# Optimization experiments

Hardware: AMD Instinct MI355X
Metric: run time of the kernel (lower is better)

The kernel has to match this reference:

```python
import jax, jax.numpy as jnp
import numpy as np

N_NODES = 50000
N_EDGES = 800000
IN_CH = 128
HID_CH = 128   # factor(2) * out_channels(64)
OUT_CH = 64


def setup_inputs() -> dict:
    key = jax.random.key(0)
    k_x, k_e, k_w1, k_w2 = jax.random.split(key, 4)
    x = jax.random.normal(k_x, (N_NODES, IN_CH), dtype=jnp.float32)
    edge_index = jax.random.randint(k_e, (2, N_EDGES), 0, N_NODES, dtype=jnp.int32)
    # GCNConv weights (Glorot) and biases, layer1: in->2*out, layer2: 2*out->out
    s1 = float(np.sqrt(6.0 / (IN_CH + HID_CH)))
    s2 = float(np.sqrt(6.0 / (HID_CH + OUT_CH)))
    W1 = jax.random.uniform(k_w1, (IN_CH, HID_CH), jnp.float32, -s1, s1)
    b1 = jnp.zeros((HID_CH,), jnp.float32)
    W2 = jax.random.uniform(k_w2, (HID_CH, OUT_CH), jnp.float32, -s2, s2)
    b2 = jnp.zeros((OUT_CH,), jnp.float32)
    return {"x": x, "edge_index": edge_index, "W1": W1, "b1": b1, "W2": W2, "b2": b2}


def reference(x, edge_index, W1, b1, W2, b2):
    N = x.shape[0]
    src, dst = edge_index[0], edge_index[1]
    # add self loops (PyG GCNConv default)
    loop = jnp.arange(N, dtype=edge_index.dtype)
    src2 = jnp.concatenate([src, loop])
    dst2 = jnp.concatenate([dst, loop])
    # symmetric normalization D^-1/2 (A+I) D^-1/2
    deg = jax.ops.segment_sum(jnp.ones_like(src2, dtype=x.dtype), dst2, num_segments=N)
    deg_inv_sqrt = jnp.where(deg > 0, jax.lax.rsqrt(jnp.maximum(deg, 1e-12)), 0.0)
    norm = deg_inv_sqrt[src2] * deg_inv_sqrt[dst2]  # [E+N]

    def gcn_conv(h, W, b):
        h = h @ W                                   # [N, C_out]
        msg = h[src2] * norm[:, None]               # gather + scale
        agg = jax.ops.segment_sum(msg, dst2, num_segments=N)  # scatter-add
        return agg + b

    h = jax.nn.relu(gcn_conv(x, W1, b1))
    h = jax.nn.relu(gcn_conv(h, W2, b2))
    return h
```

## Files before the change

kernel.cpp:

```cpp
#include <hip/hip_runtime.h>
#include <math.h>

#define NN 50000
#define NE 800000
#define NB 391
#define CAP 4096
#define CHUNK 4096

typedef __attribute__((ext_vector_type(8))) short s8v;
typedef __attribute__((ext_vector_type(8))) unsigned short u16x8;
typedef __attribute__((ext_vector_type(4))) float f4v;

__device__ inline short bf16_rtn(float f) {
  unsigned u = __builtin_bit_cast(unsigned, f);
  u = (u + 0x7FFFu + ((u >> 16) & 1u)) >> 16;
  return (short)u;
}
__device__ inline float bf16_to_f(unsigned short h) {
  unsigned u = ((unsigned)h) << 16;
  return __builtin_bit_cast(float, u);
}

__global__ __launch_bounds__(512) void k_bucketA(const int* __restrict__ src,
                                                 const int* __restrict__ dst,
                                                 int* __restrict__ bcnt,
                                                 unsigned* __restrict__ ebuf, int E) {
  __shared__ int h[NB], lofs[NB], gbase[NB], lcur[NB];
  __shared__ unsigned staged[CHUNK];
  const int tid = threadIdx.x;
  const int e0 = blockIdx.x * CHUNK;
  const int nE = min(CHUNK, E - e0);
  for (int i = tid; i < NB; i += 512) { h[i] = 0; lcur[i] = 0; }
  __syncthreads();
  for (int i = tid; i < nE; i += 512) atomicAdd(&h[dst[e0 + i] >> 7], 1);
  __syncthreads();
  if (tid < 64) {
    int carry = 0;
    for (int c = 0; c < 7; ++c) {
      int idx = c * 64 + tid;
      int v = (idx < NB) ? h[idx] : 0;
      int s = v;
#pragma unroll
      for (int o = 1; o < 64; o <<= 1) {
        int t = __shfl_up(s, o);
        if (tid >= o) s += t;
      }
      if (idx < NB) lofs[idx] = carry + s - v;
      carry += __shfl(s, 63);
    }
  }
  __syncthreads();
  for (int i = tid; i < NB; i += 512)
    gbase[i] = h[i] ? (i * CAP + atomicAdd(&bcnt[i], h[i])) : 0;
  __syncthreads();
  for (int i = tid; i < nE; i += 512) {
    int d = dst[e0 + i];
    int s = src[e0 + i];
    int b = d >> 7;
    int pos = lofs[b] + atomicAdd(&lcur[b], 1);
    staged[pos] = ((unsigned)b << 23) | ((unsigned)(d & 127) << 16) | (unsigned)s;
  }
  __syncthreads();
  for (int i = tid; i < nE; i += 512) {
    unsigned v = staged[i];
    int b = v >> 23;
    ebuf[gbase[b] + (i - lofs[b])] = v;
  }
}

__global__ __launch_bounds__(256) void k_bucketB(const unsigned* __restrict__ ebuf,
                                                 const int* __restrict__ bcnt,
                                                 unsigned short* __restrict__ col,
                                                 int* __restrict__ rps,
                                                 int* __restrict__ rpe,
                                                 float* __restrict__ dinv) {
  __shared__ int h[128], ofs[128], lc[128];
  const int tid = threadIdx.x;
  const int b = blockIdx.x;
  const int base = b * CAP;
  const int cntE = bcnt[b];
  const int node0 = b << 7;
  const int nloc = min(128, NN - node0);
  if (tid < 128) { h[tid] = 0; lc[tid] = 0; }
  __syncthreads();
  for (int i = tid; i < cntE; i += 256) atomicAdd(&h[(ebuf[base + i] >> 16) & 127], 1);
  __syncthreads();
  if (tid < 64) {
    int carry = 0;
    for (int c = 0; c < 2; ++c) {
      int idx = c * 64 + tid;
      int v = h[idx];
      int s = v;
#pragma unroll
      for (int o = 1; o < 64; o <<= 1) {
        int t = __shfl_up(s, o);
        if (tid >= o) s += t;
      }
      ofs[idx] = carry + s - v;
      carry += __shfl(s, 63);
    }
  }
  __syncthreads();
  if (tid < nloc) {
    rps[node0 + tid] = base + ofs[tid];
    rpe[node0 + tid] = base + ofs[tid] + h[tid];
    dinv[node0 + tid] = rsqrtf((float)h[tid] + 1.0f);
  }
  __syncthreads();
  for (int i = tid; i < cntE; i += 256) {
    unsigned v = ebuf[base + i];
    int l = (v >> 16) & 127;
    int p = atomicAdd(&lc[l], 1);
    col[base + ofs[l] + p] = (unsigned short)(v & 0xFFFFu);
  }
}

template <int N>
__global__ __launch_bounds__(512) void k_gemm_mfma(const float* __restrict__ X,
                                                   const float* __restrict__ W,
                                                   unsigned short* __restrict__ H,
                                                   int* __restrict__ bcnt,
                                                   int M) {
  constexpr int NT = N / 16;
  constexpr int NSLOT = 4 * NT * 64;
  __shared__ short s_hi[NSLOT * 8];
  __shared__ short s_lo[NSLOT * 8];
  const int tid = threadIdx.x;

  if (blockIdx.x == 0)
    for (int i = tid; i < NB; i += 512) bcnt[i] = 0;

  for (int slot = tid; slot < NSLOT; slot += 512) {
    int lane = slot & 63;
    int frag = slot >> 6;
    int nt = frag % NT;
    int kt = frag / NT;
    int colb = nt * 16 + (lane & 15);
    int kb = kt * 32 + (lane >> 4) * 8;
    s8v hi, lo;
#pragma unroll
    for (int j = 0; j < 8; ++j) {
      float w = W[(size_t)(kb + j) * N + colb];
      short h = bf16_rtn(w);
      hi[j] = h;
      lo[j] = bf16_rtn(w - bf16_to_f((unsigned short)h));
    }
    *(s8v*)&s_hi[slot * 8] = hi;
    *(s8v*)&s_lo[slot * 8] = lo;
  }
  __syncthreads();

  const int wave = tid >> 6, lane = tid & 63;
  const int row0 = blockIdx.x * 128 + wave * 16;
  int arow = row0 + (lane & 15);
  if (arow >= M) arow = M - 1;
  const float* xr = X + (size_t)arow * 128 + (lane >> 4) * 8;

  f4v acc[NT];
#pragma unroll
  for (int nt = 0; nt < NT; ++nt) acc[nt] = (f4v){0.f, 0.f, 0.f, 0.f};

#pragma unroll
  for (int kt = 0; kt < 4; ++kt) {
    float4 a0 = *(const float4*)(xr + kt * 32);
    float4 a1 = *(const float4*)(xr + kt * 32 + 4);
    float af[8] = {a0.x, a0.y, a0.z, a0.w, a1.x, a1.y, a1.z, a1.w};
    s8v ah, al;
#pragma unroll
    for (int j = 0; j < 8; ++j) {
      short h = bf16_rtn(af[j]);
      ah[j] = h;
      al[j] = bf16_rtn(af[j] - bf16_to_f((unsigned short)h));
    }
#pragma unroll
    for (int nt = 0; nt < NT; ++nt) {
      int base = ((kt * NT + nt) * 64 + lane) * 8;
      s8v bh = *(const s8v*)&s_hi[base];
      s8v bl = *(const s8v*)&s_lo[base];
      acc[nt] = __builtin_amdgcn_mfma_f32_16x16x32_bf16(ah, bh, acc[nt], 0, 0, 0);
      acc[nt] = __builtin_amdgcn_mfma_f32_16x16x32_bf16(ah, bl, acc[nt], 0, 0, 0);
      acc[nt] = __builtin_amdgcn_mfma_f32_16x16x32_bf16(al, bh, acc[nt], 0, 0, 0);
    }
  }

  const int orow = row0 + (lane >> 4) * 4;
  const int ocol = lane & 15;
#pragma unroll
  for (int nt = 0; nt < NT; ++nt)
#pragma unroll
    for (int r = 0; r < 4; ++r)
      if (orow + r < M)
        H[(size_t)(orow + r) * N + nt * 16 + ocol] =
            (unsigned short)bf16_rtn(acc[nt][r]);
}

__global__ __launch_bounds__(256) void k_agg1_gemm2(
    const unsigned short* __restrict__ H1, const unsigned short* __restrict__ col,
    const int* __restrict__ rps, const int* __restrict__ rpe,
    const float* __restrict__ dinv, const float* __restrict__ b1,
    const float* __restrict__ W2, unsigned short* __restrict__ H2) {
  __shared__ unsigned short s_w2[1024 * 8];
  __shared__ unsigned short s_a1[16 * 136];
  const int tid = threadIdx.x;

  for (int slot = tid; slot < 1024; slot += 256) {
    int lane = slot & 63;
    int frag = slot >> 6;
    int nt = frag & 3;
    int kt = frag >> 2;
    int colb = nt * 16 + (lane & 15);
    int kb = kt * 32 + (lane >> 4) * 8;
    u16x8 hi;
#pragma unroll
    for (int j = 0; j < 8; ++j)
      hi[j] = (unsigned short)bf16_rtn(W2[(size_t)(kb + j) * 64 + colb]);
    *(u16x8*)&s_w2[slot * 8] = hi;
  }

  const int ln = tid >> 4;
  const int node = blockIdx.x * 16 + ln;
  const int cg = (tid & 15) * 8;
  float di = dinv[node];
  float acc[8];
  u16x8 hv = *(const u16x8*)(H1 + (size_t)node * 128 + cg);
#pragma unroll
  for (int q = 0; q < 8; ++q) acc[q] = bf16_to_f(hv[q]) * di;
  int j = rps[node];
  int end = rpe[node];
  for (; j + 4 <= end; j += 4) {
    int s0 = col[j + 0], s1 = col[j + 1], s2 = col[j + 2], s3 = col[j + 3];
    float w0 = dinv[s0], w1 = dinv[s1], w2 = dinv[s2], w3 = dinv[s3];
    u16x8 a = *(const u16x8*)(H1 + (size_t)s0 * 128 + cg);
    u16x8 b = *(const u16x8*)(H1 + (size_t)s1 * 128 + cg);
    u16x8 c = *(const u16x8*)(H1 + (size_t)s2 * 128 + cg);
    u16x8 d = *(const u16x8*)(H1 + (size_t)s3 * 128 + cg);
#pragma unroll
    for (int q = 0; q < 8; ++q)
      acc[q] += bf16_to_f(a[q]) * w0 + bf16_to_f(b[q]) * w1 +
                bf16_to_f(c[q]) * w2 + bf16_to_f(d[q]) * w3;
  }
  for (; j < end; ++j) {
    int s = col[j];
    float w = dinv[s];
    u16x8 a = *(const u16x8*)(H1 + (size_t)s * 128 + cg);
#pragma unroll
    for (int q = 0; q < 8; ++q) acc[q] += bf16_to_f(a[q]) * w;
  }
  float4 bv0 = *(const float4*)(b1 + cg);
  float4 bv1 = *(const float4*)(b1 + cg + 4);
  float r[8];
  r[0] = acc[0] * di + bv0.x; r[1] = acc[1] * di + bv0.y;
  r[2] = acc[2] * di + bv0.z; r[3] = acc[3] * di + bv0.w;
  r[4] = acc[4] * di + bv1.x; r[5] = acc[5] * di + bv1.y;
  r[6] = acc[6] * di + bv1.z; r[7] = acc[7] * di + bv1.w;
  u16x8 o;
#pragma unroll
  for (int q = 0; q < 8; ++q)
    o[q] = (unsigned short)bf16_rtn(r[q] > 0.f ? r[q] : 0.f);
  *(u16x8*)&s_a1[ln * 136 + cg] = o;
  __syncthreads();

  const int wave = tid >> 6, lane = tid & 63;
  f4v cacc = (f4v){0.f, 0.f, 0.f, 0.f};
#pragma unroll
  for (int kt = 0; kt < 4; ++kt) {
    s8v ah = __builtin_bit_cast(
        s8v, *(const u16x8*)&s_a1[(lane & 15) * 136 + kt * 32 + (lane >> 4) * 8]);
    s8v bh = *(const s8v*)&s_w2[((kt * 4 + wave) * 64 + lane) * 8];
    cacc = __builtin_amdgcn_mfma_f32_16x16x32_bf16(ah, bh, cacc, 0, 0, 0);
  }
  const int node0 = blockIdx.x * 16;
  const int orow = (lane >> 4) * 4;
  const int ocol = lane & 15;
#pragma unroll
  for (int rr = 0; rr < 4; ++rr) {
    int nd = node0 + orow + rr;
    H2[(size_t)nd * 64 + wave * 16 + ocol] =
        (unsigned short)bf16_rtn(cacc[rr] * dinv[nd]);
  }
}

__global__ __launch_bounds__(256) void k_agg2(const unsigned short* __restrict__ H,
                                              const unsigned short* __restrict__ col,
                                              const int* __restrict__ rps,
                                              const int* __restrict__ rpe,
                                              const float* __restrict__ dinv,
                                              const float* __restrict__ bias,
                                              float* __restrict__ out, int n) {
  int node = blockIdx.x * 32 + threadIdx.x / 8;
  int cg = (threadIdx.x % 8) * 8;
  if (node >= n) return;
  float di = dinv[node];
  float acc[8];
  u16x8 hv = *(const u16x8*)(H + (size_t)node * 64 + cg);
#pragma unroll
  for (int q = 0; q < 8; ++q) acc[q] = bf16_to_f(hv[q]);
  int j = rps[node];
  int end = rpe[node];
  for (; j + 4 <= end; j += 4) {
    int s0 = col[j + 0], s1 = col[j + 1], s2 = col[j + 2], s3 = col[j + 3];
    u16x8 a = *(const u16x8*)(H + (size_t)s0 * 64 + cg);
    u16x8 b = *(const u16x8*)(H + (size_t)s1 * 64 + cg);
    u16x8 c = *(const u16x8*)(H + (size_t)s2 * 64 + cg);
    u16x8 d = *(const u16x8*)(H + (size_t)s3 * 64 + cg);
#pragma unroll
    for (int q = 0; q < 8; ++q)
      acc[q] += bf16_to_f(a[q]) + bf16_to_f(b[q]) + bf16_to_f(c[q]) + bf16_to_f(d[q]);
  }
  for (; j < end; ++j) {
    u16x8 a = *(const u16x8*)(H + (size_t)col[j] * 64 + cg);
#pragma unroll
    for (int q = 0; q < 8; ++q) acc[q] += bf16_to_f(a[q]);
  }
  float4 bv0 = *(const float4*)(bias + cg);
  float4 bv1 = *(const float4*)(bias + cg + 4);
  float r[8];
  r[0] = acc[0] * di + bv0.x; r[1] = acc[1] * di + bv0.y;
  r[2] = acc[2] * di + bv0.z; r[3] = acc[3] * di + bv0.w;
  r[4] = acc[4] * di + bv1.x; r[5] = acc[5] * di + bv1.y;
  r[6] = acc[6] * di + bv1.z; r[7] = acc[7] * di + bv1.w;
#pragma unroll
  for (int q = 0; q < 8; ++q) r[q] = r[q] > 0.f ? r[q] : 0.f;
  *(float4*)(out + (size_t)node * 64 + cg) = make_float4(r[0], r[1], r[2], r[3]);
  *(float4*)(out + (size_t)node * 64 + cg + 4) = make_float4(r[4], r[5], r[6], r[7]);
}

extern "C" void kernel_launch(void* const* d_in, const int* in_sizes, int n_in,
                              void* d_out, int out_size, void* d_ws, size_t ws_size,
                              hipStream_t stream) {
  const float* x  = (const float*)d_in[0];
  const int*   ei = (const int*)d_in[1];
  const float* W1 = (const float*)d_in[2];
  const float* b1 = (const float*)d_in[3];
  const float* W2 = (const float*)d_in[4];
  const float* b2 = (const float*)d_in[5];
  float* out = (float*)d_out;

  const int N = NN, E = NE;
  const int* src = ei;
  const int* dst = ei + E;

  char* ws = (char*)d_ws;
  size_t off = 0;
  auto carve = [&](size_t bytes) -> void* {
    void* p = ws + off;
    off = (off + bytes + 255) & ~(size_t)255;
    return p;
  };
  int*            bcnt = (int*)carve((size_t)NB * 4);
  unsigned short* col  = (unsigned short*)carve((size_t)NB * CAP * 2);
  int*            rps  = (int*)carve((size_t)N * 4);
  int*            rpe  = (int*)carve((size_t)N * 4);
  float*          dinv = (float*)carve((size_t)N * 4);
  unsigned short* H2   = (unsigned short*)carve((size_t)N * 64 * 2);
  unsigned short* H1   = (unsigned short*)carve((size_t)N * 128 * 2);
  unsigned*       ebuf = (unsigned*)carve((size_t)NB * CAP * 4);

  const int GB = (NN + 127) / 128;

  k_gemm_mfma<128><<<GB, 512, 0, stream>>>(x, W1, H1, bcnt, N);

  k_bucketA<<<(E + CHUNK - 1) / CHUNK, 512, 0, stream>>>(src, dst, bcnt, ebuf, E);
  k_bucketB<<<NB, 256, 0, stream>>>(ebuf, bcnt, col, rps, rpe, dinv);

  k_agg1_gemm2<<<NN / 16, 256, 0, stream>>>(H1, col, rps, rpe, dinv, b1, W2, H2);

  k_agg2<<<(N + 31) / 32, 256, 0, stream>>>(H2, col, rps, rpe, dinv, b2, out, N);
}
```

Measured before the change: 87.95 us.

## Fuse layer-1 GEMM with edge bucketing and drop global bucket atomics

Merges the first-layer MFMA GEMM and the edge bucketing pass into one launch, using a block-index split so GEMM blocks and bucketing blocks run concurrently. Bucketing blocks no longer claim space in each bucket through global atomics. Each block instead writes its locally sorted chunk together with per-bucket counts and offsets, and the second pass gathers each bucket's runs by a prefix scan and binary search into shared memory. This removes one kernel launch and the contention on the global counters, and avoids a separate zeroing step. The cost is extra per-slice metadata traffic and a larger shared-memory footprint in the fused kernel, which may reduce occupancy for the GEMM blocks.

```diff
diff --git a/kernel.cpp b/kernel.cpp
--- a/kernel.cpp
+++ b/kernel.cpp
@@ -6,6 +6,8 @@
 #define NB 391
 #define CAP 4096
 #define CHUNK 4096
+#define NSLICE 196
+#define GB 391
 
 typedef __attribute__((ext_vector_type(8))) short s8v;
 typedef __attribute__((ext_vector_type(8))) unsigned short u16x8;
@@ -21,69 +23,176 @@
   return __builtin_bit_cast(float, u);
 }
 
-__global__ __launch_bounds__(512) void k_bucketA(const int* __restrict__ src,
-                                                 const int* __restrict__ dst,
-                                                 int* __restrict__ bcnt,
-                                                 unsigned* __restrict__ ebuf, int E) {
-  __shared__ int h[NB], lofs[NB], gbase[NB], lcur[NB];
-  __shared__ unsigned staged[CHUNK];
+__global__ __launch_bounds__(512) void k_gemm1_bucketA(
+    const float* __restrict__ X, const float* __restrict__ W,
+    unsigned short* __restrict__ H,
+    const int* __restrict__ src, const int* __restrict__ dst,
+    int* __restrict__ cnts, int* __restrict__ lofsg,
+    unsigned* __restrict__ ebuf2, int M, int E) {
+  __shared__ char smem[65536];
   const int tid = threadIdx.x;
-  const int e0 = blockIdx.x * CHUNK;
-  const int nE = min(CHUNK, E - e0);
-  for (int i = tid; i < NB; i += 512) { h[i] = 0; lcur[i] = 0; }
-  __syncthreads();
-  for (int i = tid; i < nE; i += 512) atomicAdd(&h[dst[e0 + i] >> 7], 1);
-  __syncthreads();
-  if (tid < 64) {
-    int carry = 0;
-    for (int c = 0; c < 7; ++c) {
-      int idx = c * 64 + tid;
-      int v = (idx < NB) ? h[idx] : 0;
-      int s = v;
-#pragma unroll
-      for (int o = 1; o < 64; o <<= 1) {
-        int t = __shfl_up(s, o);
-        if (tid >= o) s += t;
-      }
-      if (idx < NB) lofs[idx] = carry + s - v;
-      carry += __shfl(s, 63);
-    }
-  }
-  __syncthreads();
-  for (int i = tid; i < NB; i += 512)
-    gbase[i] = h[i] ? (i * CAP + atomicAdd(&bcnt[i], h[i])) : 0;
-  __syncthreads();
-  for (int i = tid; i < nE; i += 512) {
-    int d = dst[e0 + i];
-    int s = src[e0 + i];
-    int b = d >> 7;
-    int pos = lofs[b] + atomicAdd(&lcur[b], 1);
-    staged[pos] = ((unsigned)b << 23) | ((unsigned)(d & 127) << 16) | (unsigned)s;
-  }
-  __syncthreads();
-  for (int i = tid; i < nE; i += 512) {
-    unsigned v = staged[i];
-    int b = v >> 23;
-    ebuf[gbase[b] + (i - lofs[b])] = v;
-  }
-}
-
-__global__ __launch_bounds__(256) void k_bucketB(const unsigned* __restrict__ ebuf,
-                                                 const int* __restrict__ bcnt,
+
+  if (blockIdx.x < GB) {
+    constexpr int NT = 8;
+    constexpr int NSLOT = 4 * NT * 64;
+    short* s_hi = (short*)smem;
+    short* s_lo = (short*)(smem + 32768);
+
+    for (int slot = tid; slot < NSLOT; slot += 512) {
+      int lane = slot & 63;
+      int frag = slot >> 6;
+      int nt = frag % NT;
+      int kt = frag / NT;
+      int colb = nt * 16 + (lane & 15);
+      int kb = kt * 32 + (lane >> 4) * 8;
+      s8v hi, lo;
+#pragma unroll
+      for (int j = 0; j < 8; ++j) {
+        float w = W[(size_t)(kb + j) * 128 + colb];
+        short h = bf16_rtn(w);
+        hi[j] = h;
+        lo[j] = bf16_rtn(w - bf16_to_f((unsigned short)h));
+      }
+      *(s8v*)&s_hi[slot * 8] = hi;
+      *(s8v*)&s_lo[slot * 8] = lo;
+    }
+    __syncthreads();
+
+    const int wave = tid >> 6, lane = tid & 63;
+    const int row0 = blockIdx.x * 128 + wave * 16;
+    int arow = row0 + (lane & 15);
+    if (arow >= M) arow = M - 1;
+    const float* xr = X + (size_t)arow * 128 + (lane >> 4) * 8;
+
+    f4v acc[NT];
+#pragma unroll
+    for (int nt = 0; nt < NT; ++nt) acc[nt] = (f4v){0.f, 0.f, 0.f, 0.f};
+
+#pragma unroll
+    for (int kt = 0; kt < 4; ++kt) {
+      float4 a0 = *(const float4*)(xr + kt * 32);
+      float4 a1 = *(const float4*)(xr + kt * 32 + 4);
+      float af[8] = {a0.x, a0.y, a0.z, a0.w, a1.x, a1.y, a1.z, a1.w};
+      s8v ah, al;
+#pragma unroll
+      for (int j = 0; j < 8; ++j) {
+        short h = bf16_rtn(af[j]);
+        ah[j] = h;
+        al[j] = bf16_rtn(af[j] - bf16_to_f((unsigned short)h));
+      }
+#pragma unroll
+      for (int nt = 0; nt < NT; ++nt) {
+        int base = ((kt * NT + nt) * 64 + lane) * 8;
+        s8v bh = *(const s8v*)&s_hi[base];
+        s8v bl = *(const s8v*)&s_lo[base];
+        acc[nt] = __builtin_amdgcn_mfma_f32_16x16x32_bf16(ah, bh, acc[nt], 0, 0, 0);
+        acc[nt] = __builtin_amdgcn_mfma_f32_16x16x32_bf16(ah, bl, acc[nt], 0, 0, 0);
+        acc[nt] = __builtin_amdgcn_mfma_f32_16x16x32_bf16(al, bh, acc[nt], 0, 0, 0);
+      }
+    }
+
+    const int orow = row0 + (lane >> 4) * 4;
+    const int ocol = lane & 15;
+#pragma unroll
+    for (int nt = 0; nt < NT; ++nt)
+#pragma unroll
+      for (int r = 0; r < 4; ++r)
+        if (orow + r < M)
+          H[(size_t)(orow + r) * 128 + nt * 16 + ocol] =
+              (unsigned short)bf16_rtn(acc[nt][r]);
+  } else {
+    int* h    = (int*)smem;
+    int* lofs = (int*)(smem + 1600);
+    int* lcur = (int*)(smem + 3200);
+    unsigned* staged = (unsigned*)(smem + 4800);
+    const int k = blockIdx.x - GB;
+    const int e0 = k * CHUNK;
+    const int nE = min(CHUNK, E - e0);
+    for (int i = tid; i < NB; i += 512) { h[i] = 0; lcur[i] = 0; }
+    __syncthreads();
+    for (int i = tid; i < nE; i += 512) atomicAdd(&h[dst[e0 + i] >> 7], 1);
+    __syncthreads();
+    if (tid < 64) {
+      int carry = 0;
+      for (int c = 0; c < 7; ++c) {
+        int idx = c * 64 + tid;
+        int v = (idx < NB) ? h[idx] : 0;
+        int s = v;
+#pragma unroll
+        for (int o = 1; o < 64; o <<= 1) {
+          int t = __shfl_up(s, o);
+          if (tid >= o) s += t;
+        }
+        if (idx < NB) lofs[idx] = carry + s - v;
+        carry += __shfl(s, 63);
+      }
+    }
+    __syncthreads();
+    for (int i = tid; i < nE; i += 512) {
+      int d = dst[e0 + i];
+      int s = src[e0 + i];
+      int b = d >> 7;
+      int pos = lofs[b] + atomicAdd(&lcur[b], 1);
+      staged[pos] = ((unsigned)(d & 127) << 16) | (unsigned)s;
+    }
+    __syncthreads();
+    for (int i = tid; i < nE; i += 512) ebuf2[e0 + i] = staged[i];
+    for (int i = tid; i < NB; i += 512) {
+      cnts[(size_t)k * NB + i] = h[i];
+      lofsg[(size_t)k * NB + i] = lofs[i];
+    }
+  }
+}
+
+__global__ __launch_bounds__(256) void k_bucketB(const unsigned* __restrict__ ebuf2,
+                                                 const int* __restrict__ cnts,
+                                                 const int* __restrict__ lofsg,
                                                  unsigned short* __restrict__ col,
                                                  int* __restrict__ rps,
                                                  int* __restrict__ rpe,
                                                  float* __restrict__ dinv) {
+  __shared__ int scnt[NSLICE], sofs[NSLICE], runstart[NSLICE + 1];
   __shared__ int h[128], ofs[128], lc[128];
+  __shared__ unsigned estage[CAP];
   const int tid = threadIdx.x;
   const int b = blockIdx.x;
   const int base = b * CAP;
-  const int cntE = bcnt[b];
   const int node0 = b << 7;
   const int nloc = min(128, NN - node0);
+  for (int k = tid; k < NSLICE; k += 256) {
+    scnt[k] = cnts[(size_t)k * NB + b];
+    sofs[k] = lofsg[(size_t)k * NB + b];
+  }
   if (tid < 128) { h[tid] = 0; lc[tid] = 0; }
   __syncthreads();
-  for (int i = tid; i < cntE; i += 256) atomicAdd(&h[(ebuf[base + i] >> 16) & 127], 1);
+  if (tid < 64) {
+    int carry = 0;
+    for (int c = 0; c < 4; ++c) {
+      int idx = c * 64 + tid;
+      int v = (idx < NSLICE) ? scnt[idx] : 0;
+      int s = v;
+#pragma unroll
+      for (int o = 1; o < 64; o <<= 1) {
+        int t = __shfl_up(s, o);
+        if (tid >= o) s += t;
+      }
+      if (idx < NSLICE) runstart[idx] = carry + s - v;
+      carry += __shfl(s, 63);
+    }
+    if (tid == 0) runstart[NSLICE] = carry;
+  }
+  __syncthreads();
+  const int cntE = runstart[NSLICE];
+  for (int i = tid; i < cntE; i += 256) {
+    int lo = 0, hi = NSLICE - 1;
+    while (lo < hi) {
+      int mid = (lo + hi + 1) >> 1;
+      if (runstart[mid] <= i) lo = mid; else hi = mid - 1;
+    }
+    estage[i] = ebuf2[lo * CHUNK + sofs[lo] + (i - runstart[lo])];
+  }
+  __syncthreads();
+  for (int i = tid; i < cntE; i += 256) atomicAdd(&h[(estage[i] >> 16) & 127], 1);
   __syncthreads();
   if (tid < 64) {
     int carry = 0;
@@ -108,90 +217,11 @@
   }
   __syncthreads();
   for (int i = tid; i < cntE; i += 256) {
-    unsigned v = ebuf[base + i];
+    unsigned v = estage[i];
     int l = (v >> 16) & 127;
     int p = atomicAdd(&lc[l], 1);
     col[base + ofs[l] + p] = (unsigned short)(v & 0xFFFFu);
   }
-}
-
-template <int N>
-__global__ __launch_bounds__(512) void k_gemm_mfma(const float* __restrict__ X,
-                                                   const float* __restrict__ W,
-                                                   unsigned short* __restrict__ H,
-                                                   int* __restrict__ bcnt,
-                                                   int M) {
-  constexpr int NT = N / 16;
-  constexpr int NSLOT = 4 * NT * 64;
-  __shared__ short s_hi[NSLOT * 8];
-  __shared__ short s_lo[NSLOT * 8];
-  const int tid = threadIdx.x;
-
-  if (blockIdx.x == 0)
-    for (int i = tid; i < NB; i += 512) bcnt[i] = 0;
-
-  for (int slot = tid; slot < NSLOT; slot += 512) {
-    int lane = slot & 63;
-    int frag = slot >> 6;
-    int nt = frag % NT;
-    int kt = frag / NT;
-    int colb = nt * 16 + (lane & 15);
-    int kb = kt * 32 + (lane >> 4) * 8;
-    s8v hi, lo;
-#pragma unroll
-    for (int j = 0; j < 8; ++j) {
-      float w = W[(size_t)(kb + j) * N + colb];
-      short h = bf16_rtn(w);
-      hi[j] = h;
-      lo[j] = bf16_rtn(w - bf16_to_f((unsigned short)h));
-    }
-    *(s8v*)&s_hi[slot * 8] = hi;
-    *(s8v*)&s_lo[slot * 8] = lo;
-  }
-  __syncthreads();
-
-  const int wave = tid >> 6, lane = tid & 63;
-  const int row0 = blockIdx.x * 128 + wave * 16;
-  int arow = row0 + (lane & 15);
-  if (arow >= M) arow = M - 1;
-  const float* xr = X + (size_t)arow * 128 + (lane >> 4) * 8;
-
-  f4v acc[NT];
-#pragma unroll
-  for (int nt = 0; nt < NT; ++nt) acc[nt] = (f4v){0.f, 0.f, 0.f, 0.f};
-
-#pragma unroll
-  for (int kt = 0; kt < 4; ++kt) {
-    float4 a0 = *(const float4*)(xr + kt * 32);
-    float4 a1 = *(const float4*)(xr + kt * 32 + 4);
-    float af[8] = {a0.x, a0.y, a0.z, a0.w, a1.x, a1.y, a1.z, a1.w};
-    s8v ah, al;
-#pragma unroll
-    for (int j = 0; j < 8; ++j) {
-      short h = bf16_rtn(af[j]);
-      ah[j] = h;
-      al[j] = bf16_rtn(af[j] - bf16_to_f((unsigned short)h));
-    }
-#pragma unroll
-    for (int nt = 0; nt < NT; ++nt) {
-      int base = ((kt * NT + nt) * 64 + lane) * 8;
-      s8v bh = *(const s8v*)&s_hi[base];
-      s8v bl = *(const s8v*)&s_lo[base];
-      acc[nt] = __builtin_amdgcn_mfma_f32_16x16x32_bf16(ah, bh, acc[nt], 0, 0, 0);
-      acc[nt] = __builtin_amdgcn_mfma_f32_16x16x32_bf16(ah, bl, acc[nt], 0, 0, 0);
-      acc[nt] = __builtin_amdgcn_mfma_f32_16x16x32_bf16(al, bh, acc[nt], 0, 0, 0);
-    }
-  }
-
-  const int orow = row0 + (lane >> 4) * 4;
-  const int ocol = lane & 15;
-#pragma unroll
-  for (int nt = 0; nt < NT; ++nt)
-#pragma unroll
-    for (int r = 0; r < 4; ++r)
-      if (orow + r < M)
-        H[(size_t)(orow + r) * N + nt * 16 + ocol] =
-            (unsigned short)bf16_rtn(acc[nt][r]);
 }
 
 __global__ __launch_bounds__(256) void k_agg1_gemm2(
@@ -347,21 +377,20 @@
     off = (off + bytes + 255) & ~(size_t)255;
     return p;
   };
-  int*            bcnt = (int*)carve((size_t)NB * 4);
-  unsigned short* col  = (unsigned short*)carve((size_t)NB * CAP * 2);
-  int*            rps  = (int*)carve((size_t)N * 4);
-  int*            rpe  = (int*)carve((size_t)N * 4);
-  float*          dinv = (float*)carve((size_t)N * 4);
-  unsigned short* H2   = (unsigned short*)carve((size_t)N * 64 * 2);
-  unsigned short* H1   = (unsigned short*)carve((size_t)N * 128 * 2);
-  unsigned*       ebuf = (unsigned*)carve((size_t)NB * CAP * 4);
-
-  const int GB = (NN + 127) / 128;
-
-  k_gemm_mfma<128><<<GB, 512, 0, stream>>>(x, W1, H1, bcnt, N);
-
-  k_bucketA<<<(E + CHUNK - 1) / CHUNK, 512, 0, stream>>>(src, dst, bcnt, ebuf, E);
-  k_bucketB<<<NB, 256, 0, stream>>>(ebuf, bcnt, col, rps, rpe, dinv);
+  int*            cnts  = (int*)carve((size_t)NSLICE * NB * 4);
+  int*            lofsg = (int*)carve((size_t)NSLICE * NB * 4);
+  unsigned*       ebuf2 = (unsigned*)carve((size_t)NSLICE * CHUNK * 4);
+  unsigned short* col   = (unsigned short*)carve((size_t)NB * CAP * 2);
+  int*            rps   = (int*)carve((size_t)N * 4);
+  int*            rpe   = (int*)carve((size_t)N * 4);
+  float*          dinv  = (float*)carve((size_t)N * 4);
+  unsigned short* H2    = (unsigned short*)carve((size_t)N * 64 * 2);
+  unsigned short* H1    = (unsigned short*)carve((size_t)N * 128 * 2);
+
+  k_gemm1_bucketA<<<GB + NSLICE, 512, 0, stream>>>(x, W1, H1, src, dst,
+                                                   cnts, lofsg, ebuf2, N, E);
+
+  k_bucketB<<<NB, 256, 0, stream>>>(ebuf2, cnts, lofsg, col, rps, rpe, dinv);
 
   k_agg1_gemm2<<<NN / 16, 256, 0, stream>>>(H1, col, rps, rpe, dinv, b1, W2, H2);
 
```

Measured after the change: 86.12 us. 2.1% less time.
